# Kernel tuning notes

Hardware: AMD Instinct MI355X
Metric: run time of the kernel (lower is better)

## Reference

```python
import jax, jax.numpy as jnp
import numpy as np

NB_BINS = 10
N = 33554432  # number of predictions


def setup_inputs() -> dict:
    key = jax.random.key(0)
    k1, k2 = jax.random.split(key)
    logits = jax.random.normal(k1, (N,), dtype=jnp.float32)
    labels = jax.random.randint(k2, (N,), 0, 2, dtype=jnp.int32)
    return {"logits": logits, "labels": labels}


def reference(logits, labels):
    nb = NB_BINS
    conf = jax.nn.sigmoid(logits)
    # Bin b covers (b/nb, (b+1)/nb]: conf > lower & conf <= upper.
    # ceil(conf*nb)-1 maps exact boundary k/nb to bin k-1, matching gt/le.
    # sigmoid output is strictly in (0,1) for finite logits, so clip is safe.
    bins = jnp.clip(jnp.ceil(conf * nb).astype(jnp.int32) - 1, 0, nb - 1)

    counts = jax.ops.segment_sum(jnp.ones_like(conf), bins, num_segments=nb)
    label_sum = jax.ops.segment_sum(labels.astype(conf.dtype), bins, num_segments=nb)
    conf_sum = jax.ops.segment_sum(conf, bins, num_segments=nb)

    nonempty = counts > 0
    denom = jnp.where(nonempty, counts, 1.0)
    positives_per_bin = jnp.where(nonempty, label_sum / denom, 0.0)
    confidence_per_bin = jnp.where(nonempty, conf_sum / denom, 0.0)

    ece_i = jnp.where(nonempty, jnp.abs(positives_per_bin - confidence_per_bin), 0.0)
    ece = jnp.sum(ece_i)
    max_ece = jnp.max(ece_i)  # original inits max_ece=0, zeros for empty bins match
    return positives_per_bin, confidence_per_bin, ece, max_ece
```

## Files before the change

### kernel.cpp

```cpp
#include <hip/hip_runtime.h>

#define NB 10

__device__ __forceinline__ void proc(float x, int lab, float* csum, int* pl) {
    float e = __expf(-x);
    float conf = 1.0f / (1.0f + e);
    int b = (int)ceilf(conf * 10.0f) - 1;
    b = min(max(b, 0), NB - 1);
    int packed = 1 | (lab << 16);
#pragma unroll
    for (int i = 0; i < NB; ++i) {
        bool m = (b == i);
        csum[i] += m ? conf : 0.0f;
        pl[i]   += m ? packed : 0;
    }
}

__global__ __launch_bounds__(256) void ece_partial(const float* __restrict__ logits,
                                                   const int* __restrict__ labels,
                                                   float* __restrict__ ws,
                                                   int n, int wstride) {
    float csum[NB];
    int pl[NB];
#pragma unroll
    for (int i = 0; i < NB; ++i) { csum[i] = 0.0f; pl[i] = 0; }

    const int n4 = n >> 2;
    const float4* __restrict__ l4 = (const float4*)logits;
    const int4*   __restrict__ b4 = (const int4*)labels;

    int tid = blockIdx.x * blockDim.x + threadIdx.x;
    int stride = gridDim.x * blockDim.x;
    for (int v = tid; v < n4; v += stride) {
        float4 x = l4[v];
        int4  lb = b4[v];
        proc(x.x, lb.x, csum, pl);
        proc(x.y, lb.y, csum, pl);
        proc(x.z, lb.z, csum, pl);
        proc(x.w, lb.w, csum, pl);
    }
    if (tid == 0) {
        for (int j = n4 * 4; j < n; ++j) proc(logits[j], labels[j], csum, pl);
    }

    __shared__ float lds[3 * NB];
    if (threadIdx.x < 3 * NB) lds[threadIdx.x] = 0.0f;
    __syncthreads();

    int lane = threadIdx.x & 63;
#pragma unroll
    for (int i = 0; i < NB; ++i) {
        float c = csum[i];
        int p = pl[i];
#pragma unroll
        for (int off = 32; off > 0; off >>= 1) {
            c += __shfl_down(c, off, 64);
            p += __shfl_down(p, off, 64);
        }
        if (lane == 0) {
            atomicAdd(&lds[0 * NB + i], (float)(p & 0xffff));
            atomicAdd(&lds[1 * NB + i], (float)(p >> 16));
            atomicAdd(&lds[2 * NB + i], c);
        }
    }
    __syncthreads();
    if (threadIdx.x < 3 * NB) {
        atomicAdd(&ws[threadIdx.x * wstride], lds[threadIdx.x]);
    }
}

__global__ void ece_final(const float* __restrict__ ws, float* __restrict__ out, int wstride) {
    if (threadIdx.x == 0 && blockIdx.x == 0) {
        float ece = 0.0f, mx = 0.0f;
        for (int b = 0; b < NB; ++b) {
            float cnt = ws[(0 * NB + b) * wstride];
            float ls  = ws[(1 * NB + b) * wstride];
            float cs  = ws[(2 * NB + b) * wstride];
            float pos = 0.0f, cfb = 0.0f, e = 0.0f;
            if (cnt > 0.0f) {
                pos = ls / cnt;
                cfb = cs / cnt;
                e = fabsf(pos - cfb);
            }
            out[b] = pos;
            out[NB + b] = cfb;
            ece += e;
            mx = fmaxf(mx, e);
        }
        out[2 * NB] = ece;
        out[2 * NB + 1] = mx;
    }
}

extern "C" void kernel_launch(void* const* d_in, const int* in_sizes, int n_in,
                              void* d_out, int out_size, void* d_ws, size_t ws_size,
                              hipStream_t stream) {
    const float* logits = (const float*)d_in[0];
    const int*   labels = (const int*)d_in[1];
    float* out = (float*)d_out;
    float* ws  = (float*)d_ws;
    int n = in_sizes[0];

    int wstride = (ws_size >= 30 * 16 * sizeof(float)) ? 16 : 1;

    hipMemsetAsync(d_ws, 0, (size_t)(30 * wstride) * sizeof(float), stream);

    const int block = 256;
    const int grid = 1024;
    ece_partial<<<grid, block, 0, stream>>>(logits, labels, ws, n, wstride);
    ece_final<<<1, 64, 0, stream>>>(ws, out, wstride);
}
```

Before: 300.0 us.

## Replace per-thread register bin accumulators with per-thread LDS histogram slots

Each element now does two LDS atomic adds into a thread-private slot of a shared histogram laid out [bin][thread], replacing the ten predicated register adds per element. The grid also doubles from 1024 to 2048 blocks. The aim is to cut the VALU work of the unrolled compare-and-add loop, at the cost of LDS atomic traffic and 20KB of LDS per block, which may limit occupancy. The packed count and label halves of the per-thread counters could overflow 16 bits if a thread handled more than 65535 elements, though with this grid each thread handles only 64.

```diff
diff --git a/kernel.cpp b/kernel.cpp
--- a/kernel.cpp
+++ b/kernel.cpp
@@ -1,71 +1,85 @@
 #include <hip/hip_runtime.h>
 
 #define NB 10
+#define BLOCK 256
+#define GRID 2048
 
-__device__ __forceinline__ void proc(float x, int lab, float* csum, int* pl) {
-    float e = __expf(-x);
-    float conf = 1.0f / (1.0f + e);
-    int b = (int)ceilf(conf * 10.0f) - 1;
-    b = min(max(b, 0), NB - 1);
-    int packed = 1 | (lab << 16);
-#pragma unroll
-    for (int i = 0; i < NB; ++i) {
-        bool m = (b == i);
-        csum[i] += m ? conf : 0.0f;
-        pl[i]   += m ? packed : 0;
-    }
-}
 
-__global__ __launch_bounds__(256) void ece_partial(const float* __restrict__ logits,
-                                                   const int* __restrict__ labels,
-                                                   float* __restrict__ ws,
-                                                   int n, int wstride) {
-    float csum[NB];
-    int pl[NB];
-#pragma unroll
-    for (int i = 0; i < NB; ++i) { csum[i] = 0.0f; pl[i] = 0; }
+__global__ __launch_bounds__(BLOCK) void ece_partial(const float* __restrict__ logits,
+                                                     const int* __restrict__ labels,
+                                                     float* __restrict__ ws,
+                                                     int n, int wstride) {
+    __shared__ float h[2 * NB * BLOCK];
+    float* hf = h;
+    unsigned int* hu = (unsigned int*)(h + NB * BLOCK);
+
+    const int tid = threadIdx.x;
+    for (int i = tid; i < 2 * NB * BLOCK; i += BLOCK) h[i] = 0.0f;
+    __syncthreads();
 
     const int n4 = n >> 2;
     const float4* __restrict__ l4 = (const float4*)logits;
     const int4*   __restrict__ b4 = (const int4*)labels;
 
-    int tid = blockIdx.x * blockDim.x + threadIdx.x;
-    int stride = gridDim.x * blockDim.x;
-    for (int v = tid; v < n4; v += stride) {
+    int gtid = blockIdx.x * BLOCK + tid;
+    int stride = GRID * BLOCK;
+
+    for (int v = gtid; v < n4; v += stride) {
         float4 x = l4[v];
         int4  lb = b4[v];
-        proc(x.x, lb.x, csum, pl);
-        proc(x.y, lb.y, csum, pl);
-        proc(x.z, lb.z, csum, pl);
-        proc(x.w, lb.w, csum, pl);
+#pragma unroll
+        for (int j = 0; j < 4; ++j) {
+            float xx = j == 0 ? x.x : j == 1 ? x.y : j == 2 ? x.z : x.w;
+            int   ll = j == 0 ? lb.x : j == 1 ? lb.y : j == 2 ? lb.z : lb.w;
+            float conf = 1.0f / (1.0f + __expf(-xx));
+            int b = (int)ceilf(conf * 10.0f) - 1;
+            b = min(max(b, 0), NB - 1);
+            int idx = b * BLOCK + tid;
+            atomicAdd(&hf[idx], conf);
+            atomicAdd(&hu[idx], 1u | ((unsigned)ll << 16));
+        }
     }
-    if (tid == 0) {
-        for (int j = n4 * 4; j < n; ++j) proc(logits[j], labels[j], csum, pl);
+    if (gtid == 0) {
+        for (int j = n4 * 4; j < n; ++j) {
+            float conf = 1.0f / (1.0f + __expf(-logits[j]));
+            int b = (int)ceilf(conf * 10.0f) - 1;
+            b = min(max(b, 0), NB - 1);
+            atomicAdd(&hf[b * BLOCK], conf);
+            atomicAdd(&hu[b * BLOCK], 1u | ((unsigned)labels[j] << 16));
+        }
     }
-
-    __shared__ float lds[3 * NB];
-    if (threadIdx.x < 3 * NB) lds[threadIdx.x] = 0.0f;
     __syncthreads();
 
-    int lane = threadIdx.x & 63;
+    float cf[NB];
+    unsigned int pu[NB];
 #pragma unroll
     for (int i = 0; i < NB; ++i) {
-        float c = csum[i];
-        int p = pl[i];
+        cf[i] = hf[i * BLOCK + tid];
+        pu[i] = hu[i * BLOCK + tid];
+    }
+    __syncthreads();
+    if (tid < 3 * NB) h[tid] = 0.0f;
+    __syncthreads();
+
+    const int lane = tid & 63;
+#pragma unroll
+    for (int i = 0; i < NB; ++i) {
+        float c = cf[i];
+        unsigned int p = pu[i];
 #pragma unroll
         for (int off = 32; off > 0; off >>= 1) {
             c += __shfl_down(c, off, 64);
             p += __shfl_down(p, off, 64);
         }
         if (lane == 0) {
-            atomicAdd(&lds[0 * NB + i], (float)(p & 0xffff));
-            atomicAdd(&lds[1 * NB + i], (float)(p >> 16));
-            atomicAdd(&lds[2 * NB + i], c);
+            atomicAdd(&h[0 * NB + i], (float)(p & 0xffffu));
+            atomicAdd(&h[1 * NB + i], (float)(p >> 16));
+            atomicAdd(&h[2 * NB + i], c);
         }
     }
     __syncthreads();
-    if (threadIdx.x < 3 * NB) {
-        atomicAdd(&ws[threadIdx.x * wstride], lds[threadIdx.x]);
+    if (tid < 3 * NB) {
+        atomicAdd(&ws[tid * wstride], h[tid]);
     }
 }
 
@@ -105,8 +119,6 @@
 
     hipMemsetAsync(d_ws, 0, (size_t)(30 * wstride) * sizeof(float), stream);
 
-    const int block = 256;
-    const int grid = 1024;
-    ece_partial<<<grid, block, 0, stream>>>(logits, labels, ws, n, wstride);
+    ece_partial<<<GRID, BLOCK, 0, stream>>>(logits, labels, ws, n, wstride);
     ece_final<<<1, 64, 0, stream>>>(ws, out, wstride);
 }
```

New measurement: 378.2 us. 1.26x slower.
